# Performance work log

Measured on AMD Instinct MI355X. Metric: run time of the kernel, lower is better.

Reference implementation:

```python
import jax, jax.numpy as jnp
import numpy as np

NUM_SCOPES, NUM_DECOMPS, BATCH, NUM_IN, NUM_SUMS = 32, 8, 256, 256, 256


def setup_inputs() -> dict:
    key = jax.random.key(0)
    k1, k2 = jax.random.split(key)
    # x: log-probabilities from children, shape [scopes, decomps, batch, num_nodes_in]
    x = jax.random.normal(k1, (NUM_SCOPES, NUM_DECOMPS, BATCH, NUM_IN), dtype=jnp.float32)
    # accumulators: positive weights, shape [scopes, decomps, num_nodes_in, num_sums]
    accumulators = jax.random.uniform(
        k2, (NUM_SCOPES, NUM_DECOMPS, NUM_IN, NUM_SUMS), dtype=jnp.float32,
        minval=1e-3, maxval=1.0)
    return {"x": x, "accumulators": accumulators}


def _logmatmul(x, logw):
    # out[s,d,b,j] = logsumexp_i( x[s,d,b,i] + logw[s,d,i,j] )
    # Stable form: factor out per-row / per-col maxes, do a real GEMM in linear space.
    xmax = jnp.max(x, axis=3, keepdims=True)            # [s,d,b,1]
    wmax = jnp.max(logw, axis=2, keepdims=True)         # [s,d,1,j]
    y = jnp.einsum('sdbi,sdij->sdbj', jnp.exp(x - xmax), jnp.exp(logw - wmax))
    return jnp.log(y) + xmax + wmax                     # [s,d,b,j]


def reference(x, accumulators):
    # Default path: logspace_accumulators=False, backprop_mode=GRADIENT
    log_weights = jax.nn.log_softmax(jnp.log(accumulators), axis=2)
    return _logmatmul(x, log_weights)
```

## Files before the change

### kernel.cpp

```cpp
#include <hip/hip_runtime.h>


#define NB  256
#define NI  256
#define NJ  256
#define BH  128

typedef __attribute__((ext_vector_type(8))) short bf16x8;
typedef __attribute__((ext_vector_type(4))) float f32x4;

__device__ __forceinline__ unsigned short f2bf(float f) {
  unsigned int u = __float_as_uint(f);
  u += 0x7FFFu + ((u >> 16) & 1u);
  return (unsigned short)(u >> 16);
}

__global__ __launch_bounds__(1024, 4)
void densesum_kernel(const float* __restrict__ x,
                     const float* __restrict__ acc,
                     float* __restrict__ out) {
  const int sd = blockIdx.x;
  const float* xb = x   + (size_t)sd * NB * NI;
  const float* ab = acc + (size_t)sd * NI * NJ;
  float*       ob = out + (size_t)sd * NB * NJ;

  __shared__ unsigned short As[BH * 64];
  __shared__ unsigned short Bs[NJ * NI];
  __shared__ float redbuf[8 * NJ];
  __shared__ float logS[NJ];

  const int tid  = threadIdx.x;
  const int lane = tid & 63;
  const int wid  = tid >> 6;
  const int wr   = wid >> 3;
  const int wc   = wid & 7;
  const int l15  = lane & 15;
  const int lk   = lane >> 4;
  const int r    = (lane >> 1) & 3;
  const bool s1 = (r & 1), s2 = (r & 2);
  const int kp   = wid;
  const int jbB  = lane * 4;

  f32x4 C[4][2];
  float bsum0 = 0.f, bsum1 = 0.f, bsum2 = 0.f, bsum3 = 0.f;
  float4 pa[2];
  float4 pb[4];

  auto zeroC = [&]() {
    #pragma unroll
    for (int m = 0; m < 4; ++m)
      #pragma unroll
      for (int n = 0; n < 2; ++n)
        C[m][n] = (f32x4){0.f, 0.f, 0.f, 0.f};
  };

  auto loadA = [&](const float* xh, int kc) {
    #pragma unroll
    for (int it = 0; it < 2; ++it) {
      int q  = tid + it * 1024;
      int b  = q >> 4;
      int c0 = (q & 15) * 4;
      pa[it] = *reinterpret_cast<const float4*>(xh + (size_t)b * NI + kc * 64 + c0);
    }
  };
  auto loadB = [&](int kc) {
    const float* src = ab + (size_t)(kc * 64 + kp * 4) * NJ + jbB;
    pb[0] = *reinterpret_cast<const float4*>(src);
    pb[1] = *reinterpret_cast<const float4*>(src + NJ);
    pb[2] = *reinterpret_cast<const float4*>(src + 2 * NJ);
    pb[3] = *reinterpret_cast<const float4*>(src + 3 * NJ);
  };
  auto convA = [&]() {
    #pragma unroll
    for (int it = 0; it < 2; ++it) {
      int q  = tid + it * 1024;
      int b  = q >> 4;
      int c0 = (q & 15) * 4;
      ushort4 h;
      h.x = f2bf(__expf(pa[it].x));
      h.y = f2bf(__expf(pa[it].y));
      h.z = f2bf(__expf(pa[it].z));
      h.w = f2bf(__expf(pa[it].w));
      *reinterpret_cast<ushort4*>(&As[b * 64 + (c0 ^ ((b & 7) << 3))]) = h;
    }
  };
  auto convB = [&](int kc) {
    const int kg = kc * 64 + kp * 4;
    float4 v0 = pb[0], v1 = pb[1], v2 = pb[2], v3 = pb[3];
    #define ROT(v, u0, u1, u2, u3)                                              \
      { float t0 = s1 ? v.y : v.x, t1 = s1 ? v.z : v.y,                         \
              t2 = s1 ? v.w : v.z, t3 = s1 ? v.x : v.w;                         \
        u0 = s2 ? t2 : t0; u1 = s2 ? t3 : t1;                                   \
        u2 = s2 ? t0 : t2; u3 = s2 ? t1 : t3; }
    float a00, a01, a02, a03; ROT(v0, a00, a01, a02, a03);
    float a10, a11, a12, a13; ROT(v1, a10, a11, a12, a13);
    float a20, a21, a22, a23; ROT(v2, a20, a21, a22, a23);
    float a30, a31, a32, a33; ROT(v3, a30, a31, a32, a33);
    #undef ROT
    #define STORE_COL(cc, w0, w1, w2, w3)                                       \
      { int jc = jbB + ((cc + r) & 3);                                          \
        bsum##cc += w0 + w1 + w2 + w3;                                          \
        ushort4 h; h.x = f2bf(w0); h.y = f2bf(w1);                              \
        h.z = f2bf(w2); h.w = f2bf(w3);                                         \
        *reinterpret_cast<ushort4*>(&Bs[jc * NI + (kg ^ ((jc & 7) << 3))]) = h; }
    STORE_COL(0, a00, a10, a20, a30);
    STORE_COL(1, a01, a11, a21, a31);
    STORE_COL(2, a02, a12, a22, a32);
    STORE_COL(3, a03, a13, a23, a33);
    #undef STORE_COL
  };
  auto mfmaChunk = [&](int kc) {
    #pragma unroll
    for (int ks = 0; ks < 2; ++ks) {
      const int ka = ks * 32 + 8 * lk;
      const int kg = kc * 64 + ka;
      bf16x8 bfr[2];
      #pragma unroll
      for (int n = 0; n < 2; ++n) {
        int row = wc * 32 + n * 16 + l15;
        bfr[n] = *reinterpret_cast<const bf16x8*>(&Bs[row * NI + (kg ^ ((row & 7) << 3))]);
      }
      #pragma unroll
      for (int m = 0; m < 4; ++m) {
        int row = wr * 64 + m * 16 + l15;
        bf16x8 af = *reinterpret_cast<const bf16x8*>(&As[row * 64 + (ka ^ ((row & 7) << 3))]);
        #pragma unroll
        for (int n = 0; n < 2; ++n)
          C[m][n] = __builtin_amdgcn_mfma_f32_16x16x32_bf16(af, bfr[n], C[m][n], 0, 0, 0);
      }
    }
  };
  auto epilogue = [&](int bh) {
    float* obh = ob + (size_t)bh * BH * NJ;
    #pragma unroll
    for (int m = 0; m < 4; ++m) {
      int b0 = wr * 64 + m * 16 + lk * 4;
      #pragma unroll
      for (int n = 0; n < 2; ++n) {
        int j = wc * 32 + n * 16 + l15;
        float ls = logS[j];
        #pragma unroll
        for (int rr = 0; rr < 4; ++rr) {
          obh[(size_t)(b0 + rr) * NJ + j] = __logf(C[m][n][rr]) - ls;
        }
      }
    }
  };

  loadA(xb, 0);
  loadB(0);
  zeroC();
  for (int kc = 0; kc < 4; ++kc) {
    convA();
    convB(kc);
    __syncthreads();
    if (kc < 3) {
      loadA(xb, kc + 1);
      loadB(kc + 1);
    } else {
      loadA(xb + (size_t)BH * NI, 0);
    }
    mfmaChunk(kc);
    __syncthreads();
  }

  if (wid >= 8) {
    float* row = &redbuf[(wid - 8) * NJ];
    row[jbB + ((0 + r) & 3)] = bsum0;
    row[jbB + ((1 + r) & 3)] = bsum1;
    row[jbB + ((2 + r) & 3)] = bsum2;
    row[jbB + ((3 + r) & 3)] = bsum3;
  }
  __syncthreads();
  if (wid < 8) {
    float* row = &redbuf[wid * NJ];
    row[jbB + ((0 + r) & 3)] += bsum0;
    row[jbB + ((1 + r) & 3)] += bsum1;
    row[jbB + ((2 + r) & 3)] += bsum2;
    row[jbB + ((3 + r) & 3)] += bsum3;
  }
  __syncthreads();
  if (tid < NJ) {
    float s = 0.f;
    #pragma unroll
    for (int c = 0; c < 8; ++c) s += redbuf[c * NJ + tid];
    logS[tid] = __logf(s);
  }
  __syncthreads();

  epilogue(0);

  zeroC();
  for (int kc = 0; kc < 4; ++kc) {
    convA();
    __syncthreads();
    if (kc < 3) loadA(xb + (size_t)BH * NI, kc + 1);
    mfmaChunk(kc);
    __syncthreads();
  }

  epilogue(1);
}

extern "C" void kernel_launch(void* const* d_in, const int* in_sizes, int n_in,
                              void* d_out, int out_size, void* d_ws, size_t ws_size,
                              hipStream_t stream) {
  const float* x   = (const float*)d_in[0];
  const float* acc = (const float*)d_in[1];
  float* out = (float*)d_out;
  hipLaunchKernelGGL(densesum_kernel, dim3(256), dim3(1024), 0, stream, x, acc, out);
}
```

Baseline: 39.06 us.

## Split output columns across two blocks and compute column sums via MFMA

Each (scope,decomp) is now handled by two 512-thread blocks that each own half of the output columns, giving 512 blocks instead of 256 so more CUs are filled. The per-column weight sums used for the softmax normalizer are now computed with an extra MFMA against a ones vector instead of a shared-memory reduction, which removes that reduction and its barriers. The cost is that each block re-reads and re-exponentiates the full x slab, doubling that work. The normalizer also becomes a sum of bf16-rounded weights rather than fp32 values, which slightly changes accuracy.

```diff
diff --git a/kernel.cpp b/kernel.cpp
--- a/kernel.cpp
+++ b/kernel.cpp
@@ -4,7 +4,8 @@
 #define NB  256
 #define NI  256
 #define NJ  256
-#define BH  128
+#define JH  128
+#define PH  128
 
 typedef __attribute__((ext_vector_type(8))) short bf16x8;
 typedef __attribute__((ext_vector_type(4))) float f32x4;
@@ -15,36 +16,39 @@
   return (unsigned short)(u >> 16);
 }
 
-__global__ __launch_bounds__(1024, 4)
+__global__ __launch_bounds__(512, 4)
 void densesum_kernel(const float* __restrict__ x,
                      const float* __restrict__ acc,
                      float* __restrict__ out) {
-  const int sd = blockIdx.x;
-  const float* xb = x   + (size_t)sd * NB * NI;
-  const float* ab = acc + (size_t)sd * NI * NJ;
-  float*       ob = out + (size_t)sd * NB * NJ;
-
-  __shared__ unsigned short As[BH * 64];
-  __shared__ unsigned short Bs[NJ * NI];
-  __shared__ float redbuf[8 * NJ];
-  __shared__ float logS[NJ];
+  const int bid = blockIdx.x;
+  const int sd  = bid & 255;
+  const int j0  = (bid >> 8) * JH;
+  const float* xb  = x   + (size_t)sd * NB * NI;
+  const float* xb2 = xb  + (size_t)PH * NI;
+  const float* ab  = acc + (size_t)sd * NI * NJ + j0;
+  float*       ob  = out + (size_t)sd * NB * NJ + j0;
+
+  __shared__ unsigned short As[PH * 64];
+  __shared__ unsigned short Bs[JH * NI];
 
   const int tid  = threadIdx.x;
   const int lane = tid & 63;
   const int wid  = tid >> 6;
-  const int wr   = wid >> 3;
-  const int wc   = wid & 7;
+  const int wr   = wid >> 2;
+  const int wc   = wid & 3;
   const int l15  = lane & 15;
   const int lk   = lane >> 4;
   const int r    = (lane >> 1) & 3;
   const bool s1 = (r & 1), s2 = (r & 2);
-  const int kp   = wid;
-  const int jbB  = lane * 4;
 
   f32x4 C[4][2];
-  float bsum0 = 0.f, bsum1 = 0.f, bsum2 = 0.f, bsum3 = 0.f;
-  float4 pa[2];
+  f32x4 CS[2];
+  float4 pa[4];
   float4 pb[4];
+
+  bf16x8 onesf;
+  #pragma unroll
+  for (int e = 0; e < 8; ++e) onesf[e] = (short)0x3F80;
 
   auto zeroC = [&]() {
     #pragma unroll
@@ -56,15 +60,17 @@
 
   auto loadA = [&](const float* xh, int kc) {
     #pragma unroll
-    for (int it = 0; it < 2; ++it) {
-      int q  = tid + it * 1024;
+    for (int it = 0; it < 4; ++it) {
+      int q  = tid + it * 512;
       int b  = q >> 4;
       int c0 = (q & 15) * 4;
       pa[it] = *reinterpret_cast<const float4*>(xh + (size_t)b * NI + kc * 64 + c0);
     }
   };
   auto loadB = [&](int kc) {
-    const float* src = ab + (size_t)(kc * 64 + kp * 4) * NJ + jbB;
+    int kl = (tid >> 5) * 4;
+    int jb = (tid & 31) * 4;
+    const float* src = ab + (size_t)(kc * 64 + kl) * NJ + jb;
     pb[0] = *reinterpret_cast<const float4*>(src);
     pb[1] = *reinterpret_cast<const float4*>(src + NJ);
     pb[2] = *reinterpret_cast<const float4*>(src + 2 * NJ);
@@ -72,8 +78,8 @@
   };
   auto convA = [&]() {
     #pragma unroll
-    for (int it = 0; it < 2; ++it) {
-      int q  = tid + it * 1024;
+    for (int it = 0; it < 4; ++it) {
+      int q  = tid + it * 512;
       int b  = q >> 4;
       int c0 = (q & 15) * 4;
       ushort4 h;
@@ -85,7 +91,9 @@
     }
   };
   auto convB = [&](int kc) {
-    const int kg = kc * 64 + kp * 4;
+    int kl = (tid >> 5) * 4;
+    int jb = (tid & 31) * 4;
+    int kg = kc * 64 + kl;
     float4 v0 = pb[0], v1 = pb[1], v2 = pb[2], v3 = pb[3];
     #define ROT(v, u0, u1, u2, u3)                                              \
       { float t0 = s1 ? v.y : v.x, t1 = s1 ? v.z : v.y,                         \
@@ -98,8 +106,7 @@
     float a30, a31, a32, a33; ROT(v3, a30, a31, a32, a33);
     #undef ROT
     #define STORE_COL(cc, w0, w1, w2, w3)                                       \
-      { int jc = jbB + ((cc + r) & 3);                                          \
-        bsum##cc += w0 + w1 + w2 + w3;                                          \
+      { int jc = jb + ((cc + r) & 3);                                           \
         ushort4 h; h.x = f2bf(w0); h.y = f2bf(w1);                              \
         h.z = f2bf(w2); h.w = f2bf(w3);                                         \
         *reinterpret_cast<ushort4*>(&Bs[jc * NI + (kg ^ ((jc & 7) << 3))]) = h; }
@@ -109,7 +116,7 @@
     STORE_COL(3, a03, a13, a23, a33);
     #undef STORE_COL
   };
-  auto mfmaChunk = [&](int kc) {
+  auto mfmaChunkS = [&](int kc) {
     #pragma unroll
     for (int ks = 0; ks < 2; ++ks) {
       const int ka = ks * 32 + 8 * lk;
@@ -120,6 +127,9 @@
         int row = wc * 32 + n * 16 + l15;
         bfr[n] = *reinterpret_cast<const bf16x8*>(&Bs[row * NI + (kg ^ ((row & 7) << 3))]);
       }
+      #pragma unroll
+      for (int n = 0; n < 2; ++n)
+        CS[n] = __builtin_amdgcn_mfma_f32_16x16x32_bf16(onesf, bfr[n], CS[n], 0, 0, 0);
       #pragma unroll
       for (int m = 0; m < 4; ++m) {
         int row = wr * 64 + m * 16 + l15;
@@ -130,18 +140,39 @@
       }
     }
   };
-  auto epilogue = [&](int bh) {
-    float* obh = ob + (size_t)bh * BH * NJ;
+  auto mfmaChunk = [&](int kc) {
+    #pragma unroll
+    for (int ks = 0; ks < 2; ++ks) {
+      const int ka = ks * 32 + 8 * lk;
+      const int kg = kc * 64 + ka;
+      bf16x8 bfr[2];
+      #pragma unroll
+      for (int n = 0; n < 2; ++n) {
+        int row = wc * 32 + n * 16 + l15;
+        bfr[n] = *reinterpret_cast<const bf16x8*>(&Bs[row * NI + (kg ^ ((row & 7) << 3))]);
+      }
+      #pragma unroll
+      for (int m = 0; m < 4; ++m) {
+        int row = wr * 64 + m * 16 + l15;
+        bf16x8 af = *reinterpret_cast<const bf16x8*>(&As[row * 64 + (ka ^ ((row & 7) << 3))]);
+        #pragma unroll
+        for (int n = 0; n < 2; ++n)
+          C[m][n] = __builtin_amdgcn_mfma_f32_16x16x32_bf16(af, bfr[n], C[m][n], 0, 0, 0);
+      }
+    }
+  };
+  auto epilogue = [&](int p, float ls0, float ls1) {
+    float* obp = ob + (size_t)p * PH * NJ;
     #pragma unroll
     for (int m = 0; m < 4; ++m) {
       int b0 = wr * 64 + m * 16 + lk * 4;
       #pragma unroll
       for (int n = 0; n < 2; ++n) {
         int j = wc * 32 + n * 16 + l15;
-        float ls = logS[j];
+        float ls = n ? ls1 : ls0;
         #pragma unroll
         for (int rr = 0; rr < 4; ++rr) {
-          obh[(size_t)(b0 + rr) * NJ + j] = __logf(C[m][n][rr]) - ls;
+          obp[(size_t)(b0 + rr) * NJ + j] = __logf(C[m][n][rr]) - ls;
         }
       }
     }
@@ -150,6 +181,8 @@
   loadA(xb, 0);
   loadB(0);
   zeroC();
+  CS[0] = (f32x4){0.f, 0.f, 0.f, 0.f};
+  CS[1] = (f32x4){0.f, 0.f, 0.f, 0.f};
   for (int kc = 0; kc < 4; ++kc) {
     convA();
     convB(kc);
@@ -158,48 +191,27 @@
       loadA(xb, kc + 1);
       loadB(kc + 1);
     } else {
-      loadA(xb + (size_t)BH * NI, 0);
-    }
-    mfmaChunk(kc);
+      loadA(xb2, 0);
+    }
+    mfmaChunkS(kc);
     __syncthreads();
   }
 
-  if (wid >= 8) {
-    float* row = &redbuf[(wid - 8) * NJ];
-    row[jbB + ((0 + r) & 3)] = bsum0;
-    row[jbB + ((1 + r) & 3)] = bsum1;
-    row[jbB + ((2 + r) & 3)] = bsum2;
-    row[jbB + ((3 + r) & 3)] = bsum3;
-  }
-  __syncthreads();
-  if (wid < 8) {
-    float* row = &redbuf[wid * NJ];
-    row[jbB + ((0 + r) & 3)] += bsum0;
-    row[jbB + ((1 + r) & 3)] += bsum1;
-    row[jbB + ((2 + r) & 3)] += bsum2;
-    row[jbB + ((3 + r) & 3)] += bsum3;
-  }
-  __syncthreads();
-  if (tid < NJ) {
-    float s = 0.f;
-    #pragma unroll
-    for (int c = 0; c < 8; ++c) s += redbuf[c * NJ + tid];
-    logS[tid] = __logf(s);
-  }
-  __syncthreads();
-
-  epilogue(0);
+  const float ls0 = __logf(CS[0][0]);
+  const float ls1 = __logf(CS[1][0]);
+
+  epilogue(0, ls0, ls1);
 
   zeroC();
   for (int kc = 0; kc < 4; ++kc) {
     convA();
     __syncthreads();
-    if (kc < 3) loadA(xb + (size_t)BH * NI, kc + 1);
+    if (kc < 3) loadA(xb2, kc + 1);
     mfmaChunk(kc);
     __syncthreads();
   }
 
-  epilogue(1);
+  epilogue(1, ls0, ls1);
 }
 
 extern "C" void kernel_launch(void* const* d_in, const int* in_sizes, int n_in,
@@ -208,5 +220,5 @@
   const float* x   = (const float*)d_in[0];
   const float* acc = (const float*)d_in[1];
   float* out = (float*)d_out;
-  hipLaunchKernelGGL(densesum_kernel, dim3(256), dim3(1024), 0, stream, x, acc, out);
+  hipLaunchKernelGGL(densesum_kernel, dim3(NB * 2), dim3(512), 0, stream, x, acc, out);
 }
```

Measured after the change: 38.98 us. About the same (-0.2%).
